# Kernel optimization log

Hardware: AMD Instinct MI355X
Metric: run time of the kernel (lower is better)

## Reference

```python
import jax, jax.numpy as jnp
import numpy as np

TEMPERATURE = 8.0  # sqrt(head_dim=64)


def setup_inputs() -> dict:
    key = jax.random.key(0)
    ks = jax.random.split(key, 6)
    B, H, S, D = 8, 8, 1024, 64
    shp = (B, H, S, D)
    names = ["q_r", "q_i", "k_r", "k_i", "v_r", "v_i"]
    return {n: jax.random.normal(k, shp, dtype=jnp.float32) for n, k in zip(names, ks)}


def _mag_minmax_norm(attn):
    """cvnn.MagMinMaxNorm(dim=-1): min-max normalize the magnitude along the
    last axis while preserving phase: x * (|x| - min) / ((max - min) * |x|)."""
    mag = jnp.abs(attn)                              # [B,H,Sq,Sk] real
    mn = jnp.min(mag, axis=-1, keepdims=True)
    mx = jnp.max(mag, axis=-1, keepdims=True)
    return attn * ((mag - mn) / ((mx - mn) * mag))


def reference(q_r, q_i, k_r, k_i, v_r, v_i):
    q = jax.lax.complex(q_r, q_i)
    k = jax.lax.complex(k_r, k_i)
    v = jax.lax.complex(v_r, v_i)
    # complex QK^T with temperature scaling
    attn = jnp.einsum("bhqd,bhkd->bhqk", q / TEMPERATURE, k)
    attn = _mag_minmax_norm(attn)
    # dropout is identity at inference (eval mode)
    out = jnp.einsum("bhqk,bhkd->bhqd", attn, v)
    # return real/imag stacked: [2, B, H, S, D]
    return jnp.stack([out.real, out.imag])
```

## Files before the change

kernel.cpp:

```cpp
#include <hip/hip_runtime.h>
#include <math.h>

typedef unsigned short ushort_t;
typedef __attribute__((ext_vector_type(8))) short short8;
typedef __attribute__((ext_vector_type(4))) float f32x4;
typedef __attribute__((ext_vector_type(4))) int int4v;

constexpr int S = 1024, D = 64, BH = 64;
constexpr int HALF = BH * S * D;
constexpr int KROW = 72;
constexpr int VROW = 72;
constexpr int TILE_USH = 2 * 32 * KROW + 64 * VROW;
constexpr int TILE_B = TILE_USH * 2;
constexpr size_t WS_NEED = (size_t)BH * 32 * TILE_B;

#define MFMA16(a, b, c) __builtin_amdgcn_mfma_f32_16x16x32_bf16(a, b, c, 0, 0, 0)

#if defined(__has_builtin)
#if __has_builtin(__builtin_amdgcn_cvt_pk_bf16_f32)
#define HAS_CVT_PK_BF16 1
typedef __attribute__((ext_vector_type(2))) __bf16 bf16x2_t;
__device__ __forceinline__ unsigned cvtpk(float a, float b) {
  bf16x2_t v = __builtin_amdgcn_cvt_pk_bf16_f32(a, b);
  unsigned u;
  __builtin_memcpy(&u, &v, 4);
  return u;
}
#endif
#endif
#ifndef HAS_CVT_PK_BF16
#define HAS_CVT_PK_BF16 0
__device__ __forceinline__ unsigned cvtpk(float a, float b) {
  __bf16 la = (__bf16)a, lb = (__bf16)b;
  unsigned short lo, hi;
  __builtin_memcpy(&lo, &la, 2);
  __builtin_memcpy(&hi, &lb, 2);
  return (unsigned)lo | ((unsigned)hi << 16);
}
#endif

__device__ __forceinline__ int4v pack8(float4 a, float4 b) {
  int4v r;
  r.x = (int)cvtpk(a.x, a.y);
  r.y = (int)cvtpk(a.z, a.w);
  r.z = (int)cvtpk(b.x, b.y);
  r.w = (int)cvtpk(b.z, b.w);
  return r;
}

__device__ __forceinline__ short8 twist(short8 v) {
  int4v u;
  __builtin_memcpy(&u, &v, 16);
  int4v w;
  w.x = (int)((((unsigned)u.x >> 16) | ((unsigned)u.x << 16)) ^ 0x8000u);
  w.y = (int)((((unsigned)u.y >> 16) | ((unsigned)u.y << 16)) ^ 0x8000u);
  w.z = (int)((((unsigned)u.z >> 16) | ((unsigned)u.z << 16)) ^ 0x8000u);
  w.w = (int)((((unsigned)u.w >> 16) | ((unsigned)u.w << 16)) ^ 0x8000u);
  short8 r;
  __builtin_memcpy(&r, &w, 16);
  return r;
}

__global__ __launch_bounds__(256)
void prepass_kernel(const float* __restrict__ kr, const float* __restrict__ ki,
                    const float* __restrict__ vr, const float* __restrict__ vi,
                    ushort_t* __restrict__ ws) {
  __shared__ float svr[32 * 65], svi[32 * 65];
  const int t = threadIdx.x;
  const int tile = blockIdx.x;
  const size_t gbase = (size_t)tile * (32 * D);
  ushort_t* wst = ws + (size_t)tile * TILE_USH;
  const int k = t >> 3, d0 = (t & 7) * 8;
  const int dT = t >> 2, k0 = (t & 3) * 8;

  {
    float4 a = *(const float4*)(kr + gbase + k * D + d0);
    float4 b = *(const float4*)(kr + gbase + k * D + d0 + 4);
    *(int4v*)(wst + k * KROW + d0) = pack8(a, b);
  }
  {
    float4 a = *(const float4*)(ki + gbase + k * D + d0);
    float4 b = *(const float4*)(ki + gbase + k * D + d0 + 4);
    *(int4v*)(wst + 2304 + k * KROW + d0) = pack8(a, b);
  }
  {
    float4 a = *(const float4*)(vr + gbase + k * D + d0);
    float4 b = *(const float4*)(vr + gbase + k * D + d0 + 4);
    *(float4*)&svr[k * 65 + d0] = a;
    *(float4*)&svr[k * 65 + d0 + 4] = b;
    float4 c = *(const float4*)(vi + gbase + k * D + d0);
    float4 d = *(const float4*)(vi + gbase + k * D + d0 + 4);
    *(float4*)&svi[k * 65 + d0] = c;
    *(float4*)&svi[k * 65 + d0 + 4] = d;
  }
  __syncthreads();
  {
    unsigned dws[8];
#pragma unroll
    for (int j = 0; j < 8; ++j) {
      int s = k0 + j;
      dws[j] = cvtpk(svr[s * 65 + dT], -svi[s * 65 + dT]);
    }
    ushort_t* dst = wst + 4608 + dT * VROW + 2 * k0;
    *(int4v*)dst = *(int4v*)&dws[0];
    *(int4v*)(dst + 8) = *(int4v*)&dws[4];
  }
}

__global__ __launch_bounds__(256, 2)
void cvattn_mfma(const float* __restrict__ gq_r, const float* __restrict__ gq_i,
                 const ushort_t* __restrict__ ws, float* __restrict__ gout) {
  __shared__ __attribute__((aligned(16))) char smem[2 * 18432];
  ushort_t* sB = (ushort_t*)smem;
  const int t = threadIdx.x;
  const int lane = t & 63, wave = t >> 6;
  const int m = lane & 15, quad = lane >> 4;

  const int id = blockIdx.x;
  const int bh = (id & 7) * 8 + ((id >> 3) & 7);
  const int qt = id >> 6;
  const size_t base = (size_t)bh * (S * D);

  short8 fQr[2][2], fQi[2][2], fQn[2][2];
#pragma unroll
  for (int h = 0; h < 2; ++h) {
    const int row = qt * 128 + h * 64 + wave * 16 + m;
#pragma unroll
    for (int dc = 0; dc < 2; ++dc) {
      const int d = dc * 32 + quad * 8;
      const float* pr = gq_r + base + (size_t)row * D + d;
      const float* pi = gq_i + base + (size_t)row * D + d;
      int4v vr_ = pack8(*(const float4*)pr, *(const float4*)(pr + 4));
      int4v vi_ = pack8(*(const float4*)pi, *(const float4*)(pi + 4));
      __builtin_memcpy(&fQr[h][dc], &vr_, 16);
      __builtin_memcpy(&fQi[h][dc], &vi_, 16);
      fQn[h][dc] = fQi[h][dc] ^ (short)0x8000;
    }
  }

  f32x4 aAr[2][4] = {}, aAi[2][4] = {}, aUr[2][4] = {}, aUi[2][4] = {};
  float mn2[2] = {1e30f, 1e30f}, mx2[2] = {0.f, 0.f};

  const ushort_t* wsrc = ws + (size_t)bh * 32 * TILE_USH;

  int4v pre[5];
#pragma unroll
  for (int i = 0; i < 5; ++i) {
    int idx = i * 256 + t;
    if (idx < TILE_B / 16) pre[i] = *(const int4v*)(wsrc + idx * 8);
  }
#pragma unroll
  for (int i = 0; i < 5; ++i) {
    int idx = i * 256 + t;
    if (idx < TILE_B / 16) *(int4v*)(smem + idx * 16) = pre[i];
  }
#pragma unroll
  for (int i = 0; i < 5; ++i) {
    int idx = i * 256 + t;
    if (idx < TILE_B / 16) pre[i] = *(const int4v*)(wsrc + TILE_USH + idx * 8);
  }
  __syncthreads();

  for (int kb = 0; kb < 32; ++kb) {
    const int cur = kb & 1;
    const int cbu = cur * 9216;
    const int cbd = cur * 4608;

    short8 fP0[2], fP1[2], fU0[2], fU1[2];
#pragma unroll
    for (int ks = 0; ks < 2; ++ks) {
      const int krow = ks * 16 + m;
      short8 fKr0 = *(const short8*)&sB[cbu + krow * KROW + quad * 8];
      short8 fKr1 = *(const short8*)&sB[cbu + krow * KROW + 32 + quad * 8];
      short8 fKi0 = *(const short8*)&sB[cbu + 2304 + krow * KROW + quad * 8];
      short8 fKi1 = *(const short8*)&sB[cbu + 2304 + krow * KROW + 32 + quad * 8];
#pragma unroll
      for (int h = 0; h < 2; ++h) {
        f32x4 cSr = {}, cSi = {};
        cSr = MFMA16(fKr0, fQr[h][0], cSr);
        cSr = MFMA16(fKr1, fQr[h][1], cSr);
        cSr = MFMA16(fKi0, fQn[h][0], cSr);
        cSr = MFMA16(fKi1, fQn[h][1], cSr);
        cSi = MFMA16(fKi0, fQr[h][0], cSi);
        cSi = MFMA16(fKi1, fQr[h][1], cSi);
        cSi = MFMA16(fKr0, fQi[h][0], cSi);
        cSi = MFMA16(fKr1, fQi[h][1], cSi);
        unsigned pd[4], ud[4];
#pragma unroll
        for (int r = 0; r < 4; ++r) {
          float sr = cSr[r], si = cSi[r];
          float t2 = sr * sr + si * si;
          float rq = __builtin_amdgcn_rsqf(t2);
          mn2[h] = fminf(mn2[h], t2);
          mx2[h] = fmaxf(mx2[h], t2);
          pd[r] = cvtpk(sr, si);
          ud[r] = cvtpk(sr * rq, si * rq);
        }
        if (ks == 0) { __builtin_memcpy(&fP0[h], pd, 16); __builtin_memcpy(&fU0[h], ud, 16); }
        else         { __builtin_memcpy(&fP1[h], pd, 16); __builtin_memcpy(&fU1[h], ud, 16); }
      }
    }

    if (kb + 1 < 32) {
      char* dst = smem + (cur ^ 1) * 18432;
#pragma unroll
      for (int i = 0; i < 5; ++i) {
        int idx = i * 256 + t;
        if (idx < TILE_B / 16) *(int4v*)(dst + idx * 16) = pre[i];
      }
    }
    if (kb + 2 < 32) {
      const ushort_t* g = wsrc + (size_t)(kb + 2) * TILE_USH;
#pragma unroll
      for (int i = 0; i < 5; ++i) {
        int idx = i * 256 + t;
        if (idx < TILE_B / 16) pre[i] = *(const int4v*)(g + idx * 8);
      }
    }

#pragma unroll
    for (int dt = 0; dt < 4; ++dt) {
      const unsigned* vrow = (const unsigned*)sB + cbd + 2304 + (dt * 16 + m) * 36 + quad * 4;
      short8 vre0 = *(const short8*)vrow;
      short8 vre1 = *(const short8*)(vrow + 16);
      short8 vim0 = twist(vre0);
      short8 vim1 = twist(vre1);
#pragma unroll
      for (int h = 0; h < 2; ++h) {
        aAr[h][dt] = MFMA16(fP0[h], vre0, aAr[h][dt]);
        aAr[h][dt] = MFMA16(fP1[h], vre1, aAr[h][dt]);
        aAi[h][dt] = MFMA16(fP0[h], vim0, aAi[h][dt]);
        aAi[h][dt] = MFMA16(fP1[h], vim1, aAi[h][dt]);
        aUr[h][dt] = MFMA16(fU0[h], vre0, aUr[h][dt]);
        aUr[h][dt] = MFMA16(fU1[h], vre1, aUr[h][dt]);
        aUi[h][dt] = MFMA16(fU0[h], vim0, aUi[h][dt]);
        aUi[h][dt] = MFMA16(fU1[h], vim1, aUi[h][dt]);
      }
    }
    __syncthreads();
  }

#pragma unroll
  for (int h = 0; h < 2; ++h) {
#pragma unroll
    for (int mask = 16; mask < 64; mask <<= 1) {
      mn2[h] = fminf(mn2[h], __shfl_xor(mn2[h], mask, 64));
      mx2[h] = fmaxf(mx2[h], __shfl_xor(mx2[h], mask, 64));
    }
    const float mnv = sqrtf(mn2[h]);
    const float invv = 1.0f / (sqrtf(mx2[h]) - mnv);
    const int qbase = qt * 128 + h * 64 + wave * 16 + quad * 4;
#pragma unroll
    for (int r = 0; r < 4; ++r) {
      const int src = quad * 4 + r;
      const float mnr = __shfl(mnv, src, 64);
      const float ivr = __shfl(invv, src, 64);
#pragma unroll
      for (int dt = 0; dt < 4; ++dt) {
        const int d = dt * 16 + m;
        size_t o = base + (size_t)(qbase + r) * D + d;
        gout[o] = (aAr[h][dt][r] - mnr * aUr[h][dt][r]) * ivr;
        gout[HALF + o] = (aAi[h][dt][r] - mnr * aUi[h][dt][r]) * ivr;
      }
    }
  }
}

constexpr int QT = 32, KT = 32;
constexpr int DP = D + 4;
constexpr int KP = KT + 1;

#define CDOT4(SR, SI, AR, AI, BR, BI)                              \
  SR += AR.x*BR.x + AR.y*BR.y + AR.z*BR.z + AR.w*BR.w              \
      - AI.x*BI.x - AI.y*BI.y - AI.z*BI.z - AI.w*BI.w;             \
  SI += AR.x*BI.x + AR.y*BI.y + AR.z*BI.z + AR.w*BI.w              \
      + AI.x*BR.x + AI.y*BR.y + AI.z*BR.z + AI.w*BR.w;

__global__ __launch_bounds__(256, 2)
void cvattn_fallback(const float* __restrict__ gq_r, const float* __restrict__ gq_i,
                     const float* __restrict__ gk_r, const float* __restrict__ gk_i,
                     const float* __restrict__ gv_r, const float* __restrict__ gv_i,
                     float* __restrict__ gout) {
  __shared__ float qs_r[QT][DP], qs_i[QT][DP];
  __shared__ float ks_r[KT][DP], ks_i[KT][DP];
  __shared__ float vs_r[KT][DP], vs_i[KT][DP];
  __shared__ float sc_r[QT][KP], sc_i[QT][KP], sc_m[QT][KP];
  const int t = threadIdx.x;
  const int qt2 = blockIdx.x, bh = blockIdx.y;
  const size_t base = (size_t)bh * (S * D);
  {
    const float* qr_p = gq_r + base + (size_t)qt2 * QT * D;
    const float* qi_p = gq_i + base + (size_t)qt2 * QT * D;
#pragma unroll
    for (int i = 0; i < 2; ++i) {
      int e = (t + i * 256) * 4;
      int row = e >> 6, col = e & 63;
      *(float4*)&qs_r[row][col] = *(const float4*)(qr_p + e);
      *(float4*)&qs_i[row][col] = *(const float4*)(qi_p + e);
    }
  }
  const int q0 = (t >> 4) * 2, k0 = (t & 15) * 2;
  const int rB = t >> 3, dc = (t & 7) * 8;
  float Ar[8] = {}, Ai[8] = {}, Ur[8] = {}, Ui[8] = {};
  float mn = 3.4e38f, mx = 0.0f;
  for (int kb = 0; kb < S / KT; ++kb) {
    __syncthreads();
    {
      const float* kr_p = gk_r + base + (size_t)kb * KT * D;
      const float* ki_p = gk_i + base + (size_t)kb * KT * D;
      const float* vr_p = gv_r + base + (size_t)kb * KT * D;
      const float* vi_p = gv_i + base + (size_t)kb * KT * D;
#pragma unroll
      for (int i = 0; i < 2; ++i) {
        int e = (t + i * 256) * 4;
        int row = e >> 6, col = e & 63;
        *(float4*)&ks_r[row][col] = *(const float4*)(kr_p + e);
        *(float4*)&ks_i[row][col] = *(const float4*)(ki_p + e);
        *(float4*)&vs_r[row][col] = *(const float4*)(vr_p + e);
        *(float4*)&vs_i[row][col] = *(const float4*)(vi_p + e);
      }
    }
    __syncthreads();
    {
      float s00r=0.f,s00i=0.f,s01r=0.f,s01i=0.f;
      float s10r=0.f,s10i=0.f,s11r=0.f,s11i=0.f;
#pragma unroll
      for (int d = 0; d < D; d += 4) {
        float4 a0r = *(const float4*)&qs_r[q0  ][d];
        float4 a0i = *(const float4*)&qs_i[q0  ][d];
        float4 a1r = *(const float4*)&qs_r[q0+1][d];
        float4 a1i = *(const float4*)&qs_i[q0+1][d];
        float4 b0r = *(const float4*)&ks_r[k0  ][d];
        float4 b0i = *(const float4*)&ks_i[k0  ][d];
        float4 b1r = *(const float4*)&ks_r[k0+1][d];
        float4 b1i = *(const float4*)&ks_i[k0+1][d];
        CDOT4(s00r, s00i, a0r, a0i, b0r, b0i);
        CDOT4(s01r, s01i, a0r, a0i, b1r, b1i);
        CDOT4(s10r, s10i, a1r, a1i, b0r, b0i);
        CDOT4(s11r, s11i, a1r, a1i, b1r, b1i);
      }
      s00r *= 0.125f; s00i *= 0.125f; s01r *= 0.125f; s01i *= 0.125f;
      s10r *= 0.125f; s10i *= 0.125f; s11r *= 0.125f; s11i *= 0.125f;
      sc_r[q0  ][k0  ] = s00r; sc_i[q0  ][k0  ] = s00i;
      sc_m[q0  ][k0  ] = sqrtf(s00r*s00r + s00i*s00i);
      sc_r[q0  ][k0+1] = s01r; sc_i[q0  ][k0+1] = s01i;
      sc_m[q0  ][k0+1] = sqrtf(s01r*s01r + s01i*s01i);
      sc_r[q0+1][k0  ] = s10r; sc_i[q0+1][k0  ] = s10i;
      sc_m[q0+1][k0  ] = sqrtf(s10r*s10r + s10i*s10i);
      sc_r[q0+1][k0+1] = s11r; sc_i[q0+1][k0+1] = s11i;
      sc_m[q0+1][k0+1] = sqrtf(s11r*s11r + s11i*s11i);
    }
    __syncthreads();
#pragma unroll 8
    for (int k = 0; k < KT; ++k) {
      float sr = sc_r[rB][k], si = sc_i[rB][k], mg = sc_m[rB][k];
      mn = fminf(mn, mg); mx = fmaxf(mx, mg);
      float inv = 1.0f / mg;
      float ur = sr * inv, ui = si * inv;
      float vr[8], vi[8];
      *(float4*)&vr[0] = *(const float4*)&vs_r[k][dc];
      *(float4*)&vr[4] = *(const float4*)&vs_r[k][dc + 4];
      *(float4*)&vi[0] = *(const float4*)&vs_i[k][dc];
      *(float4*)&vi[4] = *(const float4*)&vs_i[k][dc + 4];
#pragma unroll
      for (int j = 0; j < 8; ++j) {
        Ar[j] += sr * vr[j] - si * vi[j];
        Ai[j] += sr * vi[j] + si * vr[j];
        Ur[j] += ur * vr[j] - ui * vi[j];
        Ui[j] += ur * vi[j] + ui * vr[j];
      }
    }
  }
  float invspan = 1.0f / (mx - mn);
  float outr[8], outi[8];
#pragma unroll
  for (int j = 0; j < 8; ++j) {
    outr[j] = (Ar[j] - mn * Ur[j]) * invspan;
    outi[j] = (Ai[j] - mn * Ui[j]) * invspan;
  }
  size_t o = base + (size_t)(qt2 * QT + rB) * D + dc;
  *(float4*)(gout + o)            = *(float4*)&outr[0];
  *(float4*)(gout + o + 4)        = *(float4*)&outr[4];
  *(float4*)(gout + HALF + o)     = *(float4*)&outi[0];
  *(float4*)(gout + HALF + o + 4) = *(float4*)&outi[4];
}

extern "C" void kernel_launch(void* const* d_in, const int* in_sizes, int n_in,
                              void* d_out, int out_size, void* d_ws, size_t ws_size,
                              hipStream_t stream) {
  if (ws_size >= WS_NEED) {
    prepass_kernel<<<dim3(BH * 32), 256, 0, stream>>>(
        (const float*)d_in[2], (const float*)d_in[3],
        (const float*)d_in[4], (const float*)d_in[5], (ushort_t*)d_ws);
    cvattn_mfma<<<dim3(S / 128 * BH), 256, 0, stream>>>(
        (const float*)d_in[0], (const float*)d_in[1],
        (const ushort_t*)d_ws, (float*)d_out);
  } else {
    cvattn_fallback<<<dim3(S / QT, BH), 256, 0, stream>>>(
        (const float*)d_in[0], (const float*)d_in[1],
        (const float*)d_in[2], (const float*)d_in[3],
        (const float*)d_in[4], (const float*)d_in[5], (float*)d_out);
  }
}
```

Baseline: 254.2 us.

## Use direct global-to-LDS loads and halve query tile per block for occupancy

Replaces the register-staged prefetch of K/V tiles with global_load_lds async copies issued at the top of each iteration into the other LDS buffer. Each block now handles 64 query rows instead of 128, doubling the grid and raising launch bounds to 4 blocks per SM, which cuts register pressure. The QK and PV stages are interleaved per 16-key sub-block, and the K imaginary negation moves from Q to K. The tradeoff is that each K/V tile is now loaded twice as often in total, and there is no explicit wait on the async copy before the barrier.

```diff
diff --git a/kernel.cpp b/kernel.cpp
--- a/kernel.cpp
+++ b/kernel.cpp
@@ -61,6 +61,19 @@
   return r;
 }
 
+__device__ __forceinline__ void stage_tile(const ushort_t* __restrict__ g,
+                                           char* l, int t) {
+#pragma unroll
+  for (int i = 0; i < 5; ++i) {
+    const int idx = i * 256 + t;
+    if (idx < TILE_B / 16) {
+      __builtin_amdgcn_global_load_lds(
+          (const __attribute__((address_space(1))) unsigned*)(g) + idx * 4,
+          (__attribute__((address_space(3))) unsigned*)(l) + idx * 4, 16, 0, 0);
+    }
+  }
+}
+
 __global__ __launch_bounds__(256)
 void prepass_kernel(const float* __restrict__ kr, const float* __restrict__ ki,
                     const float* __restrict__ vr, const float* __restrict__ vi,
@@ -107,7 +120,7 @@
   }
 }
 
-__global__ __launch_bounds__(256, 2)
+__global__ __launch_bounds__(256, 4)
 void cvattn_mfma(const float* __restrict__ gq_r, const float* __restrict__ gq_i,
                  const ushort_t* __restrict__ ws, float* __restrict__ gout) {
   __shared__ __attribute__((aligned(16))) char smem[2 * 18432];
@@ -121,10 +134,9 @@
   const int qt = id >> 6;
   const size_t base = (size_t)bh * (S * D);
 
-  short8 fQr[2][2], fQi[2][2], fQn[2][2];
-#pragma unroll
-  for (int h = 0; h < 2; ++h) {
-    const int row = qt * 128 + h * 64 + wave * 16 + m;
+  short8 fQr[2], fQi[2];
+  {
+    const int row = qt * 64 + wave * 16 + m;
 #pragma unroll
     for (int dc = 0; dc < 2; ++dc) {
       const int d = dc * 32 + quad * 8;
@@ -132,33 +144,17 @@
       const float* pi = gq_i + base + (size_t)row * D + d;
       int4v vr_ = pack8(*(const float4*)pr, *(const float4*)(pr + 4));
       int4v vi_ = pack8(*(const float4*)pi, *(const float4*)(pi + 4));
-      __builtin_memcpy(&fQr[h][dc], &vr_, 16);
-      __builtin_memcpy(&fQi[h][dc], &vi_, 16);
-      fQn[h][dc] = fQi[h][dc] ^ (short)0x8000;
-    }
-  }
-
-  f32x4 aAr[2][4] = {}, aAi[2][4] = {}, aUr[2][4] = {}, aUi[2][4] = {};
-  float mn2[2] = {1e30f, 1e30f}, mx2[2] = {0.f, 0.f};
+      __builtin_memcpy(&fQr[dc], &vr_, 16);
+      __builtin_memcpy(&fQi[dc], &vi_, 16);
+    }
+  }
+
+  f32x4 aAr[4] = {}, aAi[4] = {}, aUr[4] = {}, aUi[4] = {};
+  float mn2 = 1e30f, mx2 = 0.f;
 
   const ushort_t* wsrc = ws + (size_t)bh * 32 * TILE_USH;
 
-  int4v pre[5];
-#pragma unroll
-  for (int i = 0; i < 5; ++i) {
-    int idx = i * 256 + t;
-    if (idx < TILE_B / 16) pre[i] = *(const int4v*)(wsrc + idx * 8);
-  }
-#pragma unroll
-  for (int i = 0; i < 5; ++i) {
-    int idx = i * 256 + t;
-    if (idx < TILE_B / 16) *(int4v*)(smem + idx * 16) = pre[i];
-  }
-#pragma unroll
-  for (int i = 0; i < 5; ++i) {
-    int idx = i * 256 + t;
-    if (idx < TILE_B / 16) pre[i] = *(const int4v*)(wsrc + TILE_USH + idx * 8);
-  }
+  stage_tile(wsrc, smem, t);
   __syncthreads();
 
   for (int kb = 0; kb < 32; ++kb) {
@@ -166,7 +162,9 @@
     const int cbu = cur * 9216;
     const int cbd = cur * 4608;
 
-    short8 fP0[2], fP1[2], fU0[2], fU1[2];
+    if (kb + 1 < 32)
+      stage_tile(wsrc + (size_t)(kb + 1) * TILE_USH, smem + (cur ^ 1) * 18432, t);
+
 #pragma unroll
     for (int ks = 0; ks < 2; ++ks) {
       const int krow = ks * 16 + m;
@@ -174,94 +172,66 @@
       short8 fKr1 = *(const short8*)&sB[cbu + krow * KROW + 32 + quad * 8];
       short8 fKi0 = *(const short8*)&sB[cbu + 2304 + krow * KROW + quad * 8];
       short8 fKi1 = *(const short8*)&sB[cbu + 2304 + krow * KROW + 32 + quad * 8];
-#pragma unroll
-      for (int h = 0; h < 2; ++h) {
-        f32x4 cSr = {}, cSi = {};
-        cSr = MFMA16(fKr0, fQr[h][0], cSr);
-        cSr = MFMA16(fKr1, fQr[h][1], cSr);
-        cSr = MFMA16(fKi0, fQn[h][0], cSr);
-        cSr = MFMA16(fKi1, fQn[h][1], cSr);
-        cSi = MFMA16(fKi0, fQr[h][0], cSi);
-        cSi = MFMA16(fKi1, fQr[h][1], cSi);
-        cSi = MFMA16(fKr0, fQi[h][0], cSi);
-        cSi = MFMA16(fKr1, fQi[h][1], cSi);
-        unsigned pd[4], ud[4];
-#pragma unroll
-        for (int r = 0; r < 4; ++r) {
-          float sr = cSr[r], si = cSi[r];
-          float t2 = sr * sr + si * si;
-          float rq = __builtin_amdgcn_rsqf(t2);
-          mn2[h] = fminf(mn2[h], t2);
-          mx2[h] = fmaxf(mx2[h], t2);
-          pd[r] = cvtpk(sr, si);
-          ud[r] = cvtpk(sr * rq, si * rq);
-        }
-        if (ks == 0) { __builtin_memcpy(&fP0[h], pd, 16); __builtin_memcpy(&fU0[h], ud, 16); }
-        else         { __builtin_memcpy(&fP1[h], pd, 16); __builtin_memcpy(&fU1[h], ud, 16); }
-      }
-    }
-
-    if (kb + 1 < 32) {
-      char* dst = smem + (cur ^ 1) * 18432;
-#pragma unroll
-      for (int i = 0; i < 5; ++i) {
-        int idx = i * 256 + t;
-        if (idx < TILE_B / 16) *(int4v*)(dst + idx * 16) = pre[i];
-      }
-    }
-    if (kb + 2 < 32) {
-      const ushort_t* g = wsrc + (size_t)(kb + 2) * TILE_USH;
-#pragma unroll
-      for (int i = 0; i < 5; ++i) {
-        int idx = i * 256 + t;
-        if (idx < TILE_B / 16) pre[i] = *(const int4v*)(g + idx * 8);
-      }
-    }
-
+      short8 fKn0 = fKi0 ^ (short)0x8000;
+      short8 fKn1 = fKi1 ^ (short)0x8000;
+      f32x4 cSr = {}, cSi = {};
+      cSr = MFMA16(fKr0, fQr[0], cSr);
+      cSr = MFMA16(fKr1, fQr[1], cSr);
+      cSr = MFMA16(fKn0, fQi[0], cSr);
+      cSr = MFMA16(fKn1, fQi[1], cSr);
+      cSi = MFMA16(fKi0, fQr[0], cSi);
+      cSi = MFMA16(fKi1, fQr[1], cSi);
+      cSi = MFMA16(fKr0, fQi[0], cSi);
+      cSi = MFMA16(fKr1, fQi[1], cSi);
+      unsigned pd[4], ud[4];
+#pragma unroll
+      for (int r = 0; r < 4; ++r) {
+        float sr = cSr[r], si = cSi[r];
+        float t2 = sr * sr + si * si;
+        float rq = __builtin_amdgcn_rsqf(t2);
+        mn2 = fminf(mn2, t2);
+        mx2 = fmaxf(mx2, t2);
+        pd[r] = cvtpk(sr, si);
+        ud[r] = cvtpk(sr * rq, si * rq);
+      }
+      short8 fP, fU;
+      __builtin_memcpy(&fP, pd, 16);
+      __builtin_memcpy(&fU, ud, 16);
+
+#pragma unroll
+      for (int dt = 0; dt < 4; ++dt) {
+        const unsigned* vrow =
+            (const unsigned*)sB + cbd + 2304 + (dt * 16 + m) * 36 + ks * 16 + quad * 4;
+        short8 vre = *(const short8*)vrow;
+        short8 vim = twist(vre);
+        aAr[dt] = MFMA16(fP, vre, aAr[dt]);
+        aAi[dt] = MFMA16(fP, vim, aAi[dt]);
+        aUr[dt] = MFMA16(fU, vre, aUr[dt]);
+        aUi[dt] = MFMA16(fU, vim, aUi[dt]);
+      }
+    }
+    __syncthreads();
+  }
+
+#pragma unroll
+  for (int mask = 16; mask < 64; mask <<= 1) {
+    mn2 = fminf(mn2, __shfl_xor(mn2, mask, 64));
+    mx2 = fmaxf(mx2, __shfl_xor(mx2, mask, 64));
+  }
+  const float mnv = sqrtf(mn2);
+  const float invv = 1.0f / (sqrtf(mx2) - mnv);
+  const int qbase = qt * 64 + wave * 16 + quad * 4;
+#pragma unroll
+  for (int r = 0; r < 4; ++r) {
+    const int src = quad * 4 + r;
+    const float mnr = __shfl(mnv, src, 64);
+    const float ivr = __shfl(invv, src, 64);
 #pragma unroll
     for (int dt = 0; dt < 4; ++dt) {
-      const unsigned* vrow = (const unsigned*)sB + cbd + 2304 + (dt * 16 + m) * 36 + quad * 4;
-      short8 vre0 = *(const short8*)vrow;
-      short8 vre1 = *(const short8*)(vrow + 16);
-      short8 vim0 = twist(vre0);
-      short8 vim1 = twist(vre1);
-#pragma unroll
-      for (int h = 0; h < 2; ++h) {
-        aAr[h][dt] = MFMA16(fP0[h], vre0, aAr[h][dt]);
-        aAr[h][dt] = MFMA16(fP1[h], vre1, aAr[h][dt]);
-        aAi[h][dt] = MFMA16(fP0[h], vim0, aAi[h][dt]);
-        aAi[h][dt] = MFMA16(fP1[h], vim1, aAi[h][dt]);
-        aUr[h][dt] = MFMA16(fU0[h], vre0, aUr[h][dt]);
-        aUr[h][dt] = MFMA16(fU1[h], vre1, aUr[h][dt]);
-        aUi[h][dt] = MFMA16(fU0[h], vim0, aUi[h][dt]);
-        aUi[h][dt] = MFMA16(fU1[h], vim1, aUi[h][dt]);
-      }
-    }
-    __syncthreads();
-  }
-
-#pragma unroll
-  for (int h = 0; h < 2; ++h) {
-#pragma unroll
-    for (int mask = 16; mask < 64; mask <<= 1) {
-      mn2[h] = fminf(mn2[h], __shfl_xor(mn2[h], mask, 64));
-      mx2[h] = fmaxf(mx2[h], __shfl_xor(mx2[h], mask, 64));
-    }
-    const float mnv = sqrtf(mn2[h]);
-    const float invv = 1.0f / (sqrtf(mx2[h]) - mnv);
-    const int qbase = qt * 128 + h * 64 + wave * 16 + quad * 4;
-#pragma unroll
-    for (int r = 0; r < 4; ++r) {
-      const int src = quad * 4 + r;
-      const float mnr = __shfl(mnv, src, 64);
-      const float ivr = __shfl(invv, src, 64);
-#pragma unroll
-      for (int dt = 0; dt < 4; ++dt) {
-        const int d = dt * 16 + m;
-        size_t o = base + (size_t)(qbase + r) * D + d;
-        gout[o] = (aAr[h][dt][r] - mnr * aUr[h][dt][r]) * ivr;
-        gout[HALF + o] = (aAi[h][dt][r] - mnr * aUi[h][dt][r]) * ivr;
-      }
+      const int d = dt * 16 + m;
+      size_t o = base + (size_t)(qbase + r) * D + d;
+      gout[o] = (aAr[dt][r] - mnr * aUr[dt][r]) * ivr;
+      gout[HALF + o] = (aAi[dt][r] - mnr * aUi[dt][r]) * ivr;
     }
   }
 }
@@ -392,7 +362,7 @@
     prepass_kernel<<<dim3(BH * 32), 256, 0, stream>>>(
         (const float*)d_in[2], (const float*)d_in[3],
         (const float*)d_in[4], (const float*)d_in[5], (ushort_t*)d_ws);
-    cvattn_mfma<<<dim3(S / 128 * BH), 256, 0, stream>>>(
+    cvattn_mfma<<<dim3(S / 64 * BH), 256, 0, stream>>>(
         (const float*)d_in[0], (const float*)d_in[1],
         (const ushort_t*)d_ws, (float*)d_out);
   } else {
```

Result: faster. 245.4 us (-3.5%).
